# Kernel tuning notes

Measured on AMD Instinct MI355X. Metric: run time of the kernel, lower is better.

Reference implementation:

```python
import jax, jax.numpy as jnp
import numpy as np

B, C, D, H, W = 2, 128, 16, 64, 64

def setup_inputs() -> dict:
    key = jax.random.key(0)
    x = jax.random.normal(key, (B, C, D, H, W), dtype=jnp.float32)
    gamma = jnp.zeros((1,), dtype=jnp.float32)
    return {"x": x, "gamma": gamma}

def reference(x, gamma):
    b, c, d, h, w = x.shape
    n = d * h * w
    q = x.reshape(b, c, n)                      # proj_query: B x C x N
    # energy = Q @ K^T where K = Q (same tensor, transposed): B x C x C
    energy = jnp.einsum('bcn,bkn->bck', q, q)
    # max-subtraction trick: energy_new = max(energy, -1) - energy, then softmax
    energy_new = jnp.max(energy, axis=-1, keepdims=True) - energy
    attention = jax.nn.softmax(energy_new, axis=-1)  # B x C x C
    out = jnp.einsum('bck,bkn->bcn', attention, q)   # AV
    out = out.reshape(b, c, d, h, w)
    return gamma * out + x
```

## Files before the change

### kernel.cpp

```cpp
#include <hip/hip_runtime.h>
#include <hip/hip_bf16.h>
#include <stdint.h>

#define BB  2
#define CC  128
#define NNN 65536

typedef __bf16 bf16x8 __attribute__((ext_vector_type(8)));
typedef float  f32x16 __attribute__((ext_vector_type(16)));

__device__ __forceinline__ uint16_t f2bf(float f) {
    uint32_t u = __float_as_uint(f);
    u = (u + 0x7fffu + ((u >> 16) & 1u)) >> 16;
    return (uint16_t)u;
}
__device__ __forceinline__ uint32_t pack2(float a, float b) {
    return (uint32_t)f2bf(a) | ((uint32_t)f2bf(b) << 16);
}

#define GCH  256
#define GST  64
#define GPAD 130

__global__ __launch_bounds__(256) void gram_kernel(const float* __restrict__ x,
        float* __restrict__ partial) {
    const int bid = blockIdx.x;
    const int b   = bid >> 8, chunk = bid & 255;
    const int n0  = chunk * GCH;
    const int t   = threadIdx.x;
    const int w = t >> 6, l = t & 63, h = l >> 5, ln = l & 31;

    __shared__ uint4 lds[2][8 * GPAD];

    const float* xb = x + (size_t)b * CC * NNN;
    const int sc = t >> 3;
    const int sg = t & 7;

    f32x16 acc[4];
#pragma unroll
    for (int j = 0; j < 4; ++j)
#pragma unroll
        for (int r = 0; r < 16; ++r) acc[j][r] = 0.0f;

    float4 va[2][4], vb[2][4];
#pragma unroll
    for (int s2 = 0; s2 < 2; ++s2)
#pragma unroll
        for (int p = 0; p < 4; ++p) {
            const float* gp = xb + (size_t)(sc + 32 * p) * NNN + n0 + s2 * GST + sg * 8;
            va[s2][p] = *(const float4*)(gp);
            vb[s2][p] = *(const float4*)(gp + 4);
        }

    for (int st = 0; st < 4; ++st) {
        const int set = st & 1;
#pragma unroll
        for (int p = 0; p < 4; ++p) {
            uint4 u;
            u.x = pack2(va[set][p].x, va[set][p].y);
            u.y = pack2(va[set][p].z, va[set][p].w);
            u.z = pack2(vb[set][p].x, vb[set][p].y);
            u.w = pack2(vb[set][p].z, vb[set][p].w);
            lds[set][sg * GPAD + sc + 32 * p] = u;
        }
        if (st + 2 < 4) {
#pragma unroll
            for (int p = 0; p < 4; ++p) {
                const float* gp = xb + (size_t)(sc + 32 * p) * NNN + n0 + (st + 2) * GST + sg * 8;
                va[set][p] = *(const float4*)(gp);
                vb[set][p] = *(const float4*)(gp + 4);
            }
        }
        __syncthreads();
#pragma unroll
        for (int s = 0; s < 4; ++s) {
            bf16x8 fa = *(const bf16x8*)&lds[set][(2 * s + h) * GPAD + 32 * w + ln];
#pragma unroll
            for (int j = 0; j < 4; ++j) {
                bf16x8 fb = *(const bf16x8*)&lds[set][(2 * s + h) * GPAD + 32 * j + ln];
                acc[j] = __builtin_amdgcn_mfma_f32_32x32x16_bf16(fa, fb, acc[j], 0, 0, 0);
            }
        }
    }

    float* pb = partial + (size_t)bid * (CC * CC);
#pragma unroll
    for (int j = 0; j < 4; ++j)
#pragma unroll
        for (int r = 0; r < 16; ++r) {
            int row = 32 * w + (r & 3) + 8 * (r >> 2) + 4 * h;
            pb[row * CC + 32 * j + ln] = acc[j][r];
        }
}

__global__ __launch_bounds__(256) void reduce_softmax_kernel(
        const float* __restrict__ partial, const float* __restrict__ gamma,
        uint16_t* __restrict__ attw) {
    const int row = blockIdx.x;
    const int b = row >> 7, i = row & 127;
    const int t = threadIdx.x;
    const int j = t & 127, ph = t >> 7;

    const float* base = partial + ((size_t)(b * 256 + ph * 128)) * (CC * CC)
                      + (size_t)i * CC + j;
    float s0=0,s1=0,s2=0,s3=0,s4=0,s5=0,s6=0,s7=0;
    for (int p = 0; p < 128; p += 8) {
        s0 += base[(size_t)(p + 0) * (CC * CC)];
        s1 += base[(size_t)(p + 1) * (CC * CC)];
        s2 += base[(size_t)(p + 2) * (CC * CC)];
        s3 += base[(size_t)(p + 3) * (CC * CC)];
        s4 += base[(size_t)(p + 4) * (CC * CC)];
        s5 += base[(size_t)(p + 5) * (CC * CC)];
        s6 += base[(size_t)(p + 6) * (CC * CC)];
        s7 += base[(size_t)(p + 7) * (CC * CC)];
    }
    const float sp = ((s0 + s1) + (s2 + s3)) + ((s4 + s5) + (s6 + s7));

    __shared__ float red[256];
    __shared__ float m[128];
    red[t] = sp; __syncthreads();
    const float e = red[j] + red[j + 128];

    if (ph == 0) m[j] = e;
    __syncthreads();
    for (int s = 64; s > 0; s >>= 1) {
        if (ph == 0 && j < s) m[j] = fmaxf(m[j], m[j + s]);
        __syncthreads();
    }
    const float M = m[0]; __syncthreads();
    const float v = M - e;
    if (ph == 0) m[j] = v;
    __syncthreads();
    for (int s = 64; s > 0; s >>= 1) {
        if (ph == 0 && j < s) m[j] = fmaxf(m[j], m[j + s]);
        __syncthreads();
    }
    const float m2 = m[0]; __syncthreads();
    const float pexp = __expf(v - m2);
    if (ph == 0) m[j] = pexp;
    __syncthreads();
    for (int s = 64; s > 0; s >>= 1) {
        if (ph == 0 && j < s) m[j] += m[j + s];
        __syncthreads();
    }
    const float sum = m[0];

    if (ph == 0)
        attw[(size_t)row * CC + j] = f2bf(gamma[0] * pexp / sum);
}

#define AVN 128

union FB8 { uint16_t u[8]; bf16x8 v; };

__global__ __launch_bounds__(256) void av_kernel(const float* __restrict__ x,
        const uint16_t* __restrict__ attw, float* __restrict__ out) {
    const int b  = blockIdx.y;
    const int n0 = blockIdx.x * AVN;
    const int t  = threadIdx.x;
    const int w = t >> 6, l = t & 63, h = l >> 5, ln = l & 31;

    __shared__ uint4    attL[16 * 128];
    __shared__ uint16_t xL[128 * 128];

    {
        const uint16_t* ab = attw + (size_t)b * CC * CC;
#pragma unroll
        for (int p = 0; p < 8; ++p) {
            int c = p * 16 + (t >> 4), g = t & 15;
            attL[g * 128 + c] = *(const uint4*)(ab + (size_t)c * CC + g * 8);
        }
    }
    {
        const int kr = t >> 1, nh = (t & 1) * 64;
        const int sw = ((kr & 8) << 2) | ((kr & 7) << 3);
        const float* xr = x + ((size_t)b * CC + kr) * NNN + n0 + nh;
#pragma unroll
        for (int i = 0; i < 8; ++i) {
            float4 a  = *(const float4*)(xr + i * 8);
            float4 bq = *(const float4*)(xr + i * 8 + 4);
            uint4 u;
            u.x = pack2(a.x, a.y);  u.y = pack2(a.z, a.w);
            u.z = pack2(bq.x, bq.y); u.w = pack2(bq.z, bq.w);
            *(uint4*)&xL[kr * 128 + ((nh + i * 8) ^ sw)] = u;
        }
    }
    __syncthreads();

    f32x16 acc[4];
#pragma unroll
    for (int jt = 0; jt < 4; ++jt)
#pragma unroll
        for (int r = 0; r < 16; ++r) acc[jt][r] = 0.0f;

#pragma unroll
    for (int s = 0; s < 8; ++s) {
        bf16x8 fa = *(const bf16x8*)&attL[(2 * s + h) * 128 + 32 * w + ln];
        const int k0 = s * 16 + h * 8;
#pragma unroll
        for (int jt = 0; jt < 4; ++jt) {
            FB8 fb;
#pragma unroll
            for (int jj = 0; jj < 8; ++jj) {
                const int k = k0 + jj;
                const int sw = ((k & 8) << 2) | ((k & 7) << 3);
                fb.u[jj] = xL[k * 128 + ((32 * jt + ln) ^ sw)];
            }
            acc[jt] = __builtin_amdgcn_mfma_f32_32x32x16_bf16(fa, fb.v, acc[jt], 0, 0, 0);
        }
    }

#pragma unroll
    for (int jt = 0; jt < 4; ++jt)
#pragma unroll
        for (int r = 0; r < 16; ++r) {
            int row = (r & 3) + 8 * (r >> 2) + 4 * h;
            size_t off = ((size_t)b * CC + 32 * w + row) * NNN + n0 + 32 * jt + ln;
            out[off] = acc[jt][r] + x[off];
        }
}

extern "C" void kernel_launch(void* const* d_in, const int* in_sizes, int n_in,
                              void* d_out, int out_size, void* d_ws, size_t ws_size,
                              hipStream_t stream) {
    const float* x     = (const float*)d_in[0];
    const float* gamma = (const float*)d_in[1];
    float* out = (float*)d_out;

    float*    partial = (float*)d_ws;
    uint16_t* att     = (uint16_t*)(partial + (size_t)512 * CC * CC);

    gram_kernel<<<BB * (NNN / GCH), 256, 0, stream>>>(x, partial);
    reduce_softmax_kernel<<<BB * CC, 256, 0, stream>>>(partial, gamma, att);
    av_kernel<<<dim3(NNN / AVN, BB), 256, 0, stream>>>(x, att, out);
}
```

Before: 153.3 us.

## Restructure AV kernel with transposed k-packed LDS layout and register-held attention

The AV kernel now handles 256 columns per block. It stores x in shared memory transposed, with 8 channels packed per uint4 and an XOR swizzle, so each MFMA B fragment becomes a single 16-byte LDS read instead of eight scalar u16 gathers. Attention fragments are loaded from global memory straight into registers instead of staging through LDS. The output loop processes one column tile at a time with a single accumulator to reduce register pressure, and launch bounds request 2 blocks per CU. One leftover line computes a redundant pack that is immediately overwritten.

After: 150.3 us. -2.0%, faster.

```diff
diff --git a/kernel.cpp b/kernel.cpp
--- a/kernel.cpp
+++ b/kernel.cpp
@@ -149,75 +149,78 @@
         attw[(size_t)row * CC + j] = f2bf(gamma[0] * pexp / sum);
 }
 
-#define AVN 128
-
-union FB8 { uint16_t u[8]; bf16x8 v; };
-
-__global__ __launch_bounds__(256) void av_kernel(const float* __restrict__ x,
+#define AVN 256
+
+__global__ __launch_bounds__(256, 2) void av_kernel(const float* __restrict__ x,
         const uint16_t* __restrict__ attw, float* __restrict__ out) {
-    const int b  = blockIdx.y;
-    const int n0 = blockIdx.x * AVN;
-    const int t  = threadIdx.x;
+    const int bid = blockIdx.x;
+    const int b   = bid >> 8;
+    const int n0  = (bid & 255) * AVN;
+    const int t   = threadIdx.x;
     const int w = t >> 6, l = t & 63, h = l >> 5, ln = l & 31;
 
-    __shared__ uint4    attL[16 * 128];
-    __shared__ uint16_t xL[128 * 128];
-
+    __shared__ uint4 xT[16 * 256];
+
+    const float* xb = x + (size_t)b * CC * NNN;
+
+#pragma unroll
+    for (int p = 0; p < 4; ++p) {
+        const int g2 = 4 * w + p;
+        float4 v[8];
+#pragma unroll
+        for (int j = 0; j < 8; ++j)
+            v[j] = *(const float4*)(xb + (size_t)(8 * g2 + j) * NNN + n0 + 4 * l);
+#pragma unroll
+        for (int i = 0; i < 4; ++i) {
+            const float* f = (const float*)v;
+            uint4 u;
+            u.x = pack2(v[0].x * 0.f + ((const float*)&v[0])[i], ((const float*)&v[1])[i]);
+            u.x = pack2(((const float*)&v[0])[i], ((const float*)&v[1])[i]);
+            u.y = pack2(((const float*)&v[2])[i], ((const float*)&v[3])[i]);
+            u.z = pack2(((const float*)&v[4])[i], ((const float*)&v[5])[i]);
+            u.w = pack2(((const float*)&v[6])[i], ((const float*)&v[7])[i]);
+            const int n  = 4 * l + i;
+            const int nA = n ^ (l & 7);
+            xT[g2 * 256 + nA] = u;
+            (void)f;
+        }
+    }
+
+    bf16x8 fa[8];
     {
-        const uint16_t* ab = attw + (size_t)b * CC * CC;
-#pragma unroll
-        for (int p = 0; p < 8; ++p) {
-            int c = p * 16 + (t >> 4), g = t & 15;
-            attL[g * 128 + c] = *(const uint4*)(ab + (size_t)c * CC + g * 8);
-        }
-    }
-    {
-        const int kr = t >> 1, nh = (t & 1) * 64;
-        const int sw = ((kr & 8) << 2) | ((kr & 7) << 3);
-        const float* xr = x + ((size_t)b * CC + kr) * NNN + n0 + nh;
-#pragma unroll
-        for (int i = 0; i < 8; ++i) {
-            float4 a  = *(const float4*)(xr + i * 8);
-            float4 bq = *(const float4*)(xr + i * 8 + 4);
-            uint4 u;
-            u.x = pack2(a.x, a.y);  u.y = pack2(a.z, a.w);
-            u.z = pack2(bq.x, bq.y); u.w = pack2(bq.z, bq.w);
-            *(uint4*)&xL[kr * 128 + ((nh + i * 8) ^ sw)] = u;
-        }
-    }
-    __syncthreads();
-
-    f32x16 acc[4];
-#pragma unroll
-    for (int jt = 0; jt < 4; ++jt)
-#pragma unroll
-        for (int r = 0; r < 16; ++r) acc[jt][r] = 0.0f;
-
-#pragma unroll
-    for (int s = 0; s < 8; ++s) {
-        bf16x8 fa = *(const bf16x8*)&attL[(2 * s + h) * 128 + 32 * w + ln];
-        const int k0 = s * 16 + h * 8;
-#pragma unroll
-        for (int jt = 0; jt < 4; ++jt) {
-            FB8 fb;
-#pragma unroll
-            for (int jj = 0; jj < 8; ++jj) {
-                const int k = k0 + jj;
-                const int sw = ((k & 8) << 2) | ((k & 7) << 3);
-                fb.u[jj] = xL[k * 128 + ((32 * jt + ln) ^ sw)];
-            }
-            acc[jt] = __builtin_amdgcn_mfma_f32_32x32x16_bf16(fa, fb.v, acc[jt], 0, 0, 0);
-        }
-    }
-
-#pragma unroll
-    for (int jt = 0; jt < 4; ++jt)
+        const uint16_t* ab = attw + ((size_t)b * CC + 32 * w + ln) * CC + h * 8;
+#pragma unroll
+        for (int s = 0; s < 8; ++s)
+            fa[s] = *(const bf16x8*)(ab + s * 16);
+    }
+    __syncthreads();
+
+#pragma unroll
+    for (int jt = 0; jt < 8; ++jt) {
+        const int n  = 32 * jt + ln;
+        const int nA = n ^ ((ln >> 2) & 7);
+
+        float xr[16];
 #pragma unroll
         for (int r = 0; r < 16; ++r) {
             int row = (r & 3) + 8 * (r >> 2) + 4 * h;
-            size_t off = ((size_t)b * CC + 32 * w + row) * NNN + n0 + 32 * jt + ln;
-            out[off] = acc[jt][r] + x[off];
-        }
+            xr[r] = xb[(size_t)(32 * w + row) * NNN + n0 + n];
+        }
+
+        f32x16 acc;
+#pragma unroll
+        for (int r = 0; r < 16; ++r) acc[r] = 0.0f;
+#pragma unroll
+        for (int s = 0; s < 8; ++s) {
+            bf16x8 fb = *(const bf16x8*)&xT[(2 * s + h) * 256 + nA];
+            acc = __builtin_amdgcn_mfma_f32_32x32x16_bf16(fa[s], fb, acc, 0, 0, 0);
+        }
+#pragma unroll
+        for (int r = 0; r < 16; ++r) {
+            int row = (r & 3) + 8 * (r >> 2) + 4 * h;
+            out[((size_t)b * CC + 32 * w + row) * NNN + n0 + n] = acc[r] + xr[r];
+        }
+    }
 }
 
 extern "C" void kernel_launch(void* const* d_in, const int* in_sizes, int n_in,
@@ -232,5 +235,5 @@
 
     gram_kernel<<<BB * (NNN / GCH), 256, 0, stream>>>(x, partial);
     reduce_softmax_kernel<<<BB * CC, 256, 0, stream>>>(partial, gamma, att);
-    av_kernel<<<dim3(NNN / AVN, BB), 256, 0, stream>>>(x, att, out);
-}
+    av_kernel<<<BB * (NNN / AVN), 256, 0, stream>>>(x, att, out);
+}
```
